# Kernel tuning notes

Hardware: AMD Instinct MI355X
Metric: run time of the kernel (lower is better)

The kernel has to match this reference:

```python
import jax, jax.numpy as jnp
import numpy as np

KERNEL = (3, 3)
STRIDE = (1, 1)
DILATION = (1, 1)
PADDING = ((1, 1), (1, 1))


def setup_inputs() -> dict:
    key = jax.random.key(0)
    k1, k2 = jax.random.split(key)
    x = jax.random.normal(k1, (4096, 4096), dtype=jnp.float32)
    weight = jax.random.normal(k2, (9,), dtype=jnp.float32)
    bias = jnp.zeros((1,), dtype=jnp.float32)
    return {"x": x, "weight": weight, "bias": bias}


def reference(x, weight, bias):
    # convNdFunc: stride_transpose=1 -> repeat_interleave is identity;
    # pad(x, padding=1, 'constant', 0); view -> sliding 3x3 windows with
    # stride 1, dilation 1 over ALL dims of x; flatten window positions;
    # func = linear: flatten(3x3) @ weight + bias -> scalar per window;
    # reshape back to (H_out, W_out).
    # im2col via patches: [1, 9, H, W] (kernel taps stacked on channel axis)
    patches = jax.lax.conv_general_dilated_patches(
        x[None, None, :, :], KERNEL, STRIDE, list(PADDING),
        rhs_dilation=DILATION)
    out = jnp.einsum('kij,k->ij', patches[0], weight) + bias[0]
    return out
```

## Files before the change

### kernel.cpp

```cpp
#include <hip/hip_runtime.h>


#define H 4096
#define W 4096
#define COLS_PER_THREAD 4
#define BLOCK 256

__global__ __launch_bounds__(BLOCK) void conv3x3_kernel(
    const float* __restrict__ x, const float* __restrict__ w9,
    const float* __restrict__ bias, float* __restrict__ out) {
    const int c = (blockIdx.x * BLOCK + threadIdx.x) * COLS_PER_THREAD;
    const int r = blockIdx.y;
    if (c >= W || r >= H) return;

    const float b = bias[0];
    float acc0 = b, acc1 = b, acc2 = b, acc3 = b;

#pragma unroll
    for (int dr = 0; dr < 3; ++dr) {
        const int rr = r + dr - 1;
        if (rr < 0 || rr >= H) continue;
        const float* row = x + (size_t)rr * W + c;
        const float4 v = *(const float4*)row;
        const float left  = (c > 0)       ? row[-1] : 0.0f;
        const float right = (c + 4 < W)   ? row[4]  : 0.0f;
        const float w0 = w9[dr * 3 + 0];
        const float w1 = w9[dr * 3 + 1];
        const float w2 = w9[dr * 3 + 2];
        acc0 = fmaf(w0, left, fmaf(w1, v.x, fmaf(w2, v.y, acc0)));
        acc1 = fmaf(w0, v.x,  fmaf(w1, v.y, fmaf(w2, v.z, acc1)));
        acc2 = fmaf(w0, v.y,  fmaf(w1, v.z, fmaf(w2, v.w, acc2)));
        acc3 = fmaf(w0, v.z,  fmaf(w1, v.w, fmaf(w2, right, acc3)));
    }

    float4 o = make_float4(acc0, acc1, acc2, acc3);
    *(float4*)(out + (size_t)r * W + c) = o;
}

extern "C" void kernel_launch(void* const* d_in, const int* in_sizes, int n_in,
                              void* d_out, int out_size, void* d_ws, size_t ws_size,
                              hipStream_t stream) {
    const float* x = (const float*)d_in[0];
    const float* w = (const float*)d_in[1];
    const float* bias = (const float*)d_in[2];
    float* out = (float*)d_out;

    dim3 block(BLOCK, 1, 1);
    dim3 grid(W / (BLOCK * COLS_PER_THREAD), H, 1);
    conv3x3_kernel<<<grid, block, 0, stream>>>(x, w, bias, out);
}
```

Baseline: 129.6 us.

## Compute four output rows per thread to reuse loaded input rows

Each thread now produces a 4x4 output tile, loading 6 input rows into registers once and reusing them across the three vertically adjacent stencil taps. Weights are hoisted into registers. This cuts per-output global/L2 load traffic (3 row loads per output row down to 1.5) and reduces the grid by 4x. It raises register use and lowers the number of blocks, which may reduce latency hiding for a kernel that was already mostly bandwidth-bound with cache-served halo rows.

```diff
diff --git a/kernel.cpp b/kernel.cpp
--- a/kernel.cpp
+++ b/kernel.cpp
@@ -4,37 +4,61 @@
 #define H 4096
 #define W 4096
 #define COLS_PER_THREAD 4
+#define ROWS_PER_THREAD 4
 #define BLOCK 256
 
 __global__ __launch_bounds__(BLOCK) void conv3x3_kernel(
     const float* __restrict__ x, const float* __restrict__ w9,
     const float* __restrict__ bias, float* __restrict__ out) {
     const int c = (blockIdx.x * BLOCK + threadIdx.x) * COLS_PER_THREAD;
-    const int r = blockIdx.y;
-    if (c >= W || r >= H) return;
+    const int r0 = blockIdx.y * ROWS_PER_THREAD;
+    if (c >= W || r0 >= H) return;
 
+    float wv[9];
+#pragma unroll
+    for (int i = 0; i < 9; ++i) wv[i] = w9[i];
     const float b = bias[0];
-    float acc0 = b, acc1 = b, acc2 = b, acc3 = b;
+
+    float4 v[6];
+    float lf[6], rt[6];
+#pragma unroll
+    for (int i = 0; i < 6; ++i) {
+        const int rr = r0 + i - 1;
+        if (rr >= 0 && rr < H) {
+            const float* row = x + (size_t)rr * W + c;
+            v[i] = *(const float4*)row;
+            lf[i] = (c > 0) ? row[-1] : 0.0f;
+            rt[i] = (c + 4 < W) ? row[4] : 0.0f;
+        } else {
+            v[i] = make_float4(0.f, 0.f, 0.f, 0.f);
+            lf[i] = 0.0f;
+            rt[i] = 0.0f;
+        }
+    }
+
+    float4 acc[4];
+#pragma unroll
+    for (int j = 0; j < 4; ++j) acc[j] = make_float4(b, b, b, b);
 
 #pragma unroll
-    for (int dr = 0; dr < 3; ++dr) {
-        const int rr = r + dr - 1;
-        if (rr < 0 || rr >= H) continue;
-        const float* row = x + (size_t)rr * W + c;
-        const float4 v = *(const float4*)row;
-        const float left  = (c > 0)       ? row[-1] : 0.0f;
-        const float right = (c + 4 < W)   ? row[4]  : 0.0f;
-        const float w0 = w9[dr * 3 + 0];
-        const float w1 = w9[dr * 3 + 1];
-        const float w2 = w9[dr * 3 + 2];
-        acc0 = fmaf(w0, left, fmaf(w1, v.x, fmaf(w2, v.y, acc0)));
-        acc1 = fmaf(w0, v.x,  fmaf(w1, v.y, fmaf(w2, v.z, acc1)));
-        acc2 = fmaf(w0, v.y,  fmaf(w1, v.z, fmaf(w2, v.w, acc2)));
-        acc3 = fmaf(w0, v.z,  fmaf(w1, v.w, fmaf(w2, right, acc3)));
+    for (int j = 0; j < 4; ++j) {
+#pragma unroll
+        for (int dr = 0; dr < 3; ++dr) {
+            const int i = j + dr;
+            const float w0 = wv[dr * 3 + 0];
+            const float w1 = wv[dr * 3 + 1];
+            const float w2 = wv[dr * 3 + 2];
+            acc[j].x = fmaf(w0, lf[i],  fmaf(w1, v[i].x, fmaf(w2, v[i].y, acc[j].x)));
+            acc[j].y = fmaf(w0, v[i].x, fmaf(w1, v[i].y, fmaf(w2, v[i].z, acc[j].y)));
+            acc[j].z = fmaf(w0, v[i].y, fmaf(w1, v[i].z, fmaf(w2, v[i].w, acc[j].z)));
+            acc[j].w = fmaf(w0, v[i].z, fmaf(w1, v[i].w, fmaf(w2, rt[i],  acc[j].w)));
+        }
     }
 
-    float4 o = make_float4(acc0, acc1, acc2, acc3);
-    *(float4*)(out + (size_t)r * W + c) = o;
+#pragma unroll
+    for (int j = 0; j < 4; ++j) {
+        *(float4*)(out + (size_t)(r0 + j) * W + c) = acc[j];
+    }
 }
 
 extern "C" void kernel_launch(void* const* d_in, const int* in_sizes, int n_in,
@@ -46,6 +70,6 @@
     float* out = (float*)d_out;
 
     dim3 block(BLOCK, 1, 1);
-    dim3 grid(W / (BLOCK * COLS_PER_THREAD), H, 1);
+    dim3 grid(W / (BLOCK * COLS_PER_THREAD), H / ROWS_PER_THREAD, 1);
     conv3x3_kernel<<<grid, block, 0, stream>>>(x, w, bias, out);
 }
```

Result: faster. 121.7 us (-6.1%).
